# Kernel optimization log

Measured on AMD Instinct MI355X. Metric: run time of the kernel, lower is better.

Reference implementation:

```python
import jax, jax.numpy as jnp
import numpy as np

N_NODES = 50000
N_EDGES = 800000
CH = 128
N_GRAPHS = 8
ADD_TO_EDGE_SCORE = 0.5


def edge_scores(x, row, col, lin_w, lin_b, n):
    """Raw edge score via Linear([x_row||x_col]) then scatter-softmax over col."""
    C = x.shape[1]
    # split-weight form of cat([x[row], x[col]]) @ W^T + b (avoids the [E,2C] concat)
    raw = x[row] @ lin_w[0, :C] + x[col] @ lin_w[0, C:] + lin_b[0]  # [E]
    mx = jax.ops.segment_max(raw, col, num_segments=n)
    ex = jnp.exp(raw - mx[col])
    den = jax.ops.segment_sum(ex, col, num_segments=n)
    return ex / (den[col] + 1e-16) + ADD_TO_EDGE_SCORE


def greedy_match_cluster(row_np, col_np, score_np, n):
    """Greedy maximal matching in descending-score order + 2-element clustering."""
    perm = np.argsort(-score_np)
    rows = row_np.tolist()
    cols = col_np.tolist()
    used = np.zeros(n, dtype=bool)
    match = np.zeros(len(rows), dtype=bool)
    for e in perm.tolist():
        r = rows[e]
        c = cols[e]
        if not (used[r] or used[c]):
            match[e] = True
            used[r] = True
            used[c] = True
    cluster = np.arange(n)
    cluster[col_np[match]] = row_np[match]
    _, cluster = np.unique(cluster, return_inverse=True)
    return match, cluster


def setup_inputs() -> dict:
    key = jax.random.key(0)
    k1, k2, k3, k4, k5 = jax.random.split(key, 5)
    x = jax.random.normal(k1, (N_NODES, CH), dtype=jnp.float32)
    edge_index = jax.random.randint(k2, (2, N_EDGES), 0, N_NODES)
    batch = jnp.sort(jax.random.randint(k3, (N_NODES,), 0, N_GRAPHS))
    bound = 1.0 / np.sqrt(2 * CH)
    lin_w = jax.random.uniform(k4, (1, 2 * CH), minval=-bound, maxval=bound, dtype=jnp.float32)
    lin_b = jax.random.uniform(k5, (1,), minval=-bound, maxval=bound, dtype=jnp.float32)
    return {"x": x, "edge_index": edge_index, "batch": batch, "lin_w": lin_w, "lin_b": lin_b}


def reference(x, edge_index, batch, lin_w, lin_b):
    n = x.shape[0]
    row, col = edge_index[0], edge_index[1]
    score = edge_scores(x, row, col, lin_w, lin_b, n)  # [E]

    # sequential greedy matching / cluster relabeling (host side, non-differentiable)
    row_np, col_np = np.asarray(row), np.asarray(col)
    match, cluster_np = greedy_match_cluster(row_np, col_np, np.asarray(score), n)
    c = int(cluster_np.max()) + 1
    match_idx = jnp.asarray(np.nonzero(match)[0])
    cluster = jnp.asarray(cluster_np, dtype=jnp.int32)

    # pooled features scaled by the contracted edge's score (1.0 for singletons)
    new_x = jax.ops.segment_sum(x, cluster, num_segments=c)  # [c, C]
    root = cluster[row[match_idx]]
    new_edge_score = jnp.ones((c,), x.dtype).at[root].set(score[match_idx])
    new_x = new_x * new_edge_score[:, None]

    # coalesce(cluster[edge_index]): sort + dedup
    lin_idx = cluster_np[row_np].astype(np.int64) * c + cluster_np[col_np]
    uniq = np.unique(lin_idx)
    new_edge_index = jnp.asarray(np.stack([uniq // c, uniq % c]).astype(np.int32))

    new_batch = jnp.zeros((c,), dtype=batch.dtype).at[cluster].set(batch)
    return new_x, new_edge_index, new_batch, new_edge_score, cluster
```

## Files before the change

### kernel.cpp

```cpp
#include <hip/hip_runtime.h>

typedef unsigned int u32;
typedef unsigned short u16;
typedef unsigned long long u64;

#define CH_ 128

__device__ __forceinline__ u32 f2ord(float f){
  u32 u = __float_as_uint(f);
  return ((int)u < 0) ? ~u : (u | 0x80000000u);
}
__device__ __forceinline__ float ord2f(u32 u){
  return (u & 0x80000000u) ? __uint_as_float(u & 0x7FFFFFFFu) : __uint_as_float(~u);
}
__device__ __forceinline__ u32 ldu32(const u32* p){
  return __hip_atomic_load(p, __ATOMIC_RELAXED, __HIP_MEMORY_SCOPE_AGENT);
}
__device__ __forceinline__ void stu32(u32* p, u32 v){
  __hip_atomic_store(p, v, __ATOMIC_RELAXED, __HIP_MEMORY_SCOPE_AGENT);
}

__global__ void k_init(u32* hdr, u32* mxbits, double* den, u64* sw,
                       int* craw, int* medge, u32* deg, u32* acur,
                       u32* wpos, u32* offarr, u32 ucap, int N, int E){
  int i0 = blockIdx.x*blockDim.x + threadIdx.x;
  int nt = gridDim.x*blockDim.x;
  for (int v = i0; v < N; v += nt){
    mxbits[v]=0u; den[v]=0.0; sw[v]=0ull; craw[v]=v; medge[v]=-1;
    deg[v]=0u; acur[v]=0u; wpos[v]=0u;
    if (ucap) offarr[v] = (u32)v * ucap;
  }
  if (i0 == 0){
    for (int i = 0; i < 64; i++) hdr[i] = 0u;
    hdr[6] = (u32)N;
    offarr[N] = ucap ? (u32)N*ucap : (u32)(2*E);
  }
}

__global__ void k_dots(const float* __restrict__ x, const float* __restrict__ lw,
                       float* __restrict__ s, float* __restrict__ t, int N){
  int wid = threadIdx.x >> 6, lane = threadIdx.x & 63;
  int node = blockIdx.x*4 + wid;
  if (node >= N) return;
  const float* xr = x + (size_t)node*CH_;
  float xa = xr[lane], xb = xr[64+lane];
  float sv = xa*lw[lane]      + xb*lw[64+lane];
  float tv = xa*lw[128+lane]  + xb*lw[192+lane];
  #pragma unroll
  for (int m = 1; m < 64; m <<= 1){ sv += __shfl_xor(sv, m); tv += __shfl_xor(tv, m); }
  if (lane == 0){ s[node]=sv; t[node]=tv; }
}

__global__ void k_rawmax(const float* __restrict__ s, const float* __restrict__ t,
                         const int* __restrict__ row, const int* __restrict__ col,
                         const float* __restrict__ lb, float* __restrict__ rawex,
                         u32* __restrict__ mxbits, u32* __restrict__ rc,
                         u32* __restrict__ deg, u32 ucap, int E){
  float b = lb[0];
  int i0 = blockIdx.x*blockDim.x + threadIdx.x;
  int nt = gridDim.x*blockDim.x;
  for (int e = i0; e < E; e += nt){
    int r = row[e], c = col[e];
    float raw = (s[r] + t[c]) + b;
    rawex[e] = raw;
    atomicMax(&mxbits[c], f2ord(raw));
    rc[e] = ((u32)r << 16) | (u32)c;
    if (!ucap){
      atomicAdd(&deg[r], 1u);
      atomicAdd(&deg[c], 1u);
    }
  }
}

__global__ void k_exden(const int* __restrict__ col, const u32* __restrict__ mxbits,
                        float* __restrict__ rawex, double* __restrict__ den, int E){
  int i0 = blockIdx.x*blockDim.x + threadIdx.x;
  int nt = gridDim.x*blockDim.x;
  for (int e = i0; e < E; e += nt){
    int c = col[e];
    float ex = expf(rawex[e] - ord2f(mxbits[c]));
    rawex[e] = ex;
    atomicAdd(&den[c], (double)ex);
  }
}

__global__ void k_score(const int* __restrict__ col, float* __restrict__ rawex,
                        const double* __restrict__ den, int E){
  int i0 = blockIdx.x*blockDim.x + threadIdx.x;
  int nt = gridDim.x*blockDim.x;
  for (int e = i0; e < E; e += nt)
    rawex[e] = rawex[e]/(float)den[col[e]] + 0.5f;
}

__global__ void scan_p1(const u32* __restrict__ in, u32* __restrict__ out,
                        u32* __restrict__ bsums, const u32* __restrict__ nptr){
  __shared__ u32 sh[256];
  u32 n = *nptr;
  int t = threadIdx.x;
  u32 i = blockIdx.x*256u + (u32)t;
  u32 v = (i < n) ? in[i] : 0u;
  sh[t] = v; __syncthreads();
  for (int o = 1; o < 256; o <<= 1){
    u32 a = (t >= o) ? sh[t-o] : 0u;
    __syncthreads();
    sh[t] += a;
    __syncthreads();
  }
  if (i < n) out[i] = sh[t] - v;
  if (t == 255) bsums[blockIdx.x] = sh[255];
}
__global__ void scan_p2(u32* bsums, u32* total){
  __shared__ u32 sh[256];
  int t = threadIdx.x;
  u32 v = bsums[t];
  sh[t] = v; __syncthreads();
  for (int o = 1; o < 256; o <<= 1){
    u32 a = (t >= o) ? sh[t-o] : 0u;
    __syncthreads();
    sh[t] += a;
    __syncthreads();
  }
  bsums[t] = sh[t] - v;
  if (t == 255 && total) *total = sh[255];
}
__global__ void scan_p3(u32* out, const u32* __restrict__ bsums, const u32* __restrict__ nptr){
  u32 n = *nptr;
  u32 i = blockIdx.x*256u + threadIdx.x;
  if (i < n) out[i] += bsums[blockIdx.x];
}

__global__ void __launch_bounds__(256)
k_scoreadj(const u32* __restrict__ rc, const float* __restrict__ score,
           const u32* __restrict__ offarr, u32* __restrict__ acur,
           u64* __restrict__ adj, u16* __restrict__ adjp,
           u32 ucap, int ce, int E, int N){
  int xcd   = blockIdx.x & 7;
  int chunk = blockIdx.x >> 3;
  int vspan = (N + 7) >> 3;
  int vlo = xcd * vspan;
  int vhi = vlo + vspan; if (vhi > N) vhi = N;
  int ebeg = chunk * ce;
  int eend = ebeg + ce; if (eend > E) eend = E;
  for (int e = ebeg + threadIdx.x; e < eend; e += blockDim.x){
    u32 pk = rc[e];
    int r = (int)(pk >> 16), c = (int)(pk & 0xFFFFu);
    bool wr = (r >= vlo) & (r < vhi);
    bool wc = (c >= vlo) & (c < vhi);
    if (wr | wc){
      u64 k = ((u64)__float_as_uint(score[e]) << 20) | (u64)(0xFFFFFu - (u32)e);
      if (wr){
        u32 slot = atomicAdd(&acur[r], 1u);
        if (!ucap || slot < ucap){
          u32 pr = offarr[r] + slot;
          adj[pr] = k; adjp[pr] = (u16)c;
        }
      }
      if (wc){
        u32 slot = atomicAdd(&acur[c], 1u);
        if (!ucap || slot < ucap){
          u32 pc = offarr[c] + slot;
          adj[pc] = k; adjp[pc] = (u16)r;
        }
      }
    }
  }
}

__global__ void k_adjsort(const u32* __restrict__ offarr, const u32* __restrict__ acur,
                          u64* __restrict__ adj, u16* __restrict__ adjp,
                          u32 ucap, int N){
  __shared__ u64 shk[512];
  __shared__ u32 shp[512];
  int lane = threadIdx.x;
  u32 capn = ucap ? ucap : 0xFFFFFFFFu;
  for (int seg = blockIdx.x; seg < N; seg += gridDim.x){
    u32 base = offarr[seg];
    u32 cnt = acur[seg]; if (cnt > capn) cnt = capn;
    int n = (int)cnt;
    if (n <= 1) continue;
    if (n <= 64){
      u64 v = (lane < n) ? adj[base + lane] : 0ull;
      u32 pr = (lane < n) ? (u32)adjp[base + lane] : 0u;
      #pragma unroll
      for (int k2 = 2; k2 <= 64; k2 <<= 1)
        for (int j = k2 >> 1; j > 0; j >>= 1){
          u64 pv = __shfl_xor(v, j);
          u32 pp = (u32)__shfl_xor((int)pr, j);
          bool up  = ((lane & k2) == 0);
          bool low = ((lane & j) == 0);
          bool take_mx = (up == low);
          bool swap = take_mx ? (pv > v) : (pv < v);
          if (swap){ v = pv; pr = pp; }
        }
      if (lane < n){ adj[base + lane] = v; adjp[base + lane] = (u16)pr; }
    } else {
      int msz = 128; while (msz < n) msz <<= 1;
      for (int i = lane; i < msz; i += 64){
        shk[i] = (i < n) ? adj[base + i] : 0ull;
        shp[i] = (i < n) ? (u32)adjp[base + i] : 0u;
      }
      __syncthreads();
      for (int k2 = 2; k2 <= msz; k2 <<= 1){
        for (int j = k2 >> 1; j > 0; j >>= 1){
          for (int i = lane; i < msz; i += 64){
            int ix = i ^ j;
            if (ix > i){
              u64 a = shk[i], b2 = shk[ix];
              bool desc = ((i & k2) == 0);
              if (desc ? (a < b2) : (a > b2)){
                shk[i] = b2; shk[ix] = a;
                u32 t2 = shp[i]; shp[i] = shp[ix]; shp[ix] = t2;
              }
            }
          }
          __syncthreads();
        }
      }
      for (int i = lane; i < n; i += 64){ adj[base+i] = shk[i]; adjp[base+i] = (u16)shp[i]; }
      __syncthreads();
    }
  }
}

__global__ void k_suitor(const u32* __restrict__ rc, const u32* __restrict__ offarr,
                         const u32* __restrict__ acur,
                         const u64* __restrict__ adj, const u16* __restrict__ adjp,
                         u64* sw, u32* wpos, u32 ucap, int N){
  int i0 = blockIdx.x*blockDim.x + threadIdx.x;
  int nt = gridDim.x*blockDim.x;
  u32 capn = ucap ? ucap : 0xFFFFFFFFu;
  for (int v0 = i0; v0 < N; v0 += nt){
    u32 u = (u32)v0;
    u32 pos = offarr[u];
    u32 cnt = acur[u]; if (cnt > capn) cnt = capn;
    u32 end = pos + cnt;
    while (pos < end){
      u64 k = adj[pos];
      u32 v = (u32)adjp[pos];
      pos++;
      if (sw[v] >= k) continue;
      stu32(&wpos[u], pos);
      u64 old = atomicMax((unsigned long long*)&sw[v], (unsigned long long)k);
      if (old >= k) continue;
      if (old == 0ull) break;
      u32 e2 = 0xFFFFFu - (u32)(old & 0xFFFFFu);
      u32 p2 = rc[e2];
      u = ((p2 >> 16) == v) ? (p2 & 0xFFFFu) : (p2 >> 16);
      u32 st = offarr[u];
      u32 c2 = acur[u]; if (c2 > capn) c2 = capn;
      end = st + c2;
      u32 wp = ldu32(&wpos[u]);
      pos = (wp > st) ? wp : st;
    }
  }
}

__global__ void k_exroot(const u64* __restrict__ sw, const u32* __restrict__ rc,
                         int* __restrict__ craw, int* __restrict__ medge,
                         u32* __restrict__ rf, int N){
  int v = blockIdx.x*blockDim.x + threadIdx.x;
  if (v >= N) return;
  u64 k = sw[v];
  bool iscol = false;
  if (k != 0ull){
    u32 e = 0xFFFFFu - (u32)(k & 0xFFFFFu);
    u32 p = rc[e]; u32 r = p >> 16, c = p & 0xFFFFu;
    if ((u32)v == c && sw[r] == k){
      craw[c] = (int)r; medge[r] = (int)e;
      iscol = (r != c);
    }
  }
  rf[v] = iscol ? 0u : 1u;
}

__global__ void k_clusterzero(const int* __restrict__ craw, const u32* __restrict__ newid,
                              int* __restrict__ clout, float* __restrict__ out, size_t offC,
                              u32* __restrict__ hist, u32* __restrict__ cur2,
                              u32* __restrict__ uniqcnt, int N, int M){
  int i = blockIdx.x*blockDim.x + threadIdx.x;
  if (i < M){ hist[i]=0u; cur2[i]=0u; uniqcnt[i]=0u; }
  if (i < N){
    int cl = (int)newid[craw[i]];
    clout[i] = cl;
    out[offC + i] = (float)cl;
  }
}

__global__ void k_hist(const int* __restrict__ row, const int* __restrict__ clout,
                       u32* __restrict__ hist, int E){
  int i0 = blockIdx.x*blockDim.x + threadIdx.x;
  int nt = gridDim.x*blockDim.x;
  for (int e = i0; e < E; e += nt) atomicAdd(&hist[clout[row[e]]], 1u);
}

__global__ void k_scatter(const int* __restrict__ row, const int* __restrict__ col,
                          const int* __restrict__ clout, const u32* __restrict__ segoff,
                          u32* __restrict__ cur2, u32* __restrict__ ccbuf,
                          const u32* __restrict__ hdr, int E){
  const int P = 4;
  int cnum = (int)hdr[2];
  int span = (cnum + P - 1) / P;
  int i0 = blockIdx.x*blockDim.x + threadIdx.x;
  int nt = gridDim.x*blockDim.x;
  for (int p = 0; p < P; p++){
    int lo = p*span;
    int hi = lo + span; if (hi > cnum) hi = cnum;
    for (int e = i0; e < E; e += nt){
      int cr = clout[row[e]];
      if (cr < lo || cr >= hi) continue;
      u32 pos = segoff[cr] + atomicAdd(&cur2[cr], 1u);
      ccbuf[pos] = (u32)clout[col[e]];
    }
  }
}

__global__ void k_segsort(const u32* __restrict__ hdr, const u32* __restrict__ hist,
                          const u32* __restrict__ segoff, u32* __restrict__ ccbuf,
                          u32* __restrict__ uniqcnt){
  int c = (int)hdr[2];
  __shared__ u32 sh[1024];
  int lane = threadIdx.x;
  for (int seg = blockIdx.x; seg < c; seg += gridDim.x){
    int n = (int)hist[seg];
    if (n <= 0){ if (lane == 0) uniqcnt[seg] = 0u; continue; }
    u32 off = segoff[seg];
    if (n <= 64){
      u32 v = (lane < n) ? ccbuf[off + lane] : 0xFFFFFFFFu;
      #pragma unroll
      for (int k = 2; k <= 64; k <<= 1)
        for (int j = k >> 1; j > 0; j >>= 1){
          u32 p = __shfl_xor(v, j);
          bool up  = ((lane & k) == 0);
          bool low = ((lane & j) == 0);
          u32 mn = v < p ? v : p, mx = v < p ? p : v;
          v = (up == low) ? mn : mx;
        }
      u32 pv = __shfl_up(v, 1);
      bool un = (lane < n) && (lane == 0 || v != pv);
      u64 bal = __ballot(un);
      int cnt = __popcll(bal);
      int rk  = __popcll(bal & ((1ull << lane) - 1ull));
      if (un) ccbuf[off + rk] = v;
      if (lane == 0) uniqcnt[seg] = (u32)cnt;
    } else {
      int nn = n > 1024 ? 1024 : n;
      for (int i = lane; i < nn; i += 64) sh[i] = ccbuf[off + i];
      __syncthreads();
      for (int p = 0; p < nn; p++){
        int st = p & 1;
        for (int i = lane; 2*i + 1 + st < nn; i += 64){
          int a = 2*i + st;
          u32 x0 = sh[a], x1 = sh[a+1];
          if (x0 > x1){ sh[a] = x1; sh[a+1] = x0; }
        }
        __syncthreads();
      }
      if (lane == 0){
        int cnt = 0; u32 prev = 0u;
        for (int i = 0; i < nn; i++){
          u32 xv = sh[i];
          if (i == 0 || xv != prev){ ccbuf[off + cnt] = xv; cnt++; prev = xv; }
        }
        uniqcnt[seg] = (u32)cnt;
      }
      __syncthreads();
    }
  }
}

__global__ void k_out(const u32* __restrict__ hdr, const u32* __restrict__ segoff,
                      const u32* __restrict__ uniqcnt, const u32* __restrict__ uniqoff,
                      const u32* __restrict__ ccbuf, const int* __restrict__ craw,
                      const u32* __restrict__ newid, const int* __restrict__ medge,
                      const int* __restrict__ row, const int* __restrict__ col,
                      const float* __restrict__ score, const int* __restrict__ batch,
                      const float* __restrict__ x, float* __restrict__ out, int N){
  int c = (int)hdr[2]; u32 Ep = hdr[3];
  size_t base = (size_t)c * CH_;
  size_t offB = base + 2ull * (size_t)Ep;
  size_t offS = offB + (size_t)c;
  int gw   = (blockIdx.x*blockDim.x + threadIdx.x) >> 6;
  int lane = threadIdx.x & 63;
  int nw   = (gridDim.x*blockDim.x) >> 6;
  for (int seg = gw; seg < c; seg += nw){
    int cnt = (int)uniqcnt[seg];
    u32 so = segoff[seg], uo = uniqoff[seg];
    for (int j = lane; j < cnt; j += 64){
      u32 cc = ccbuf[so + j];
      out[base + uo + j]              = (float)seg;
      out[base + (size_t)Ep + uo + j] = (float)cc;
    }
  }
  for (int i = gw; i < N; i += nw){
    if (craw[i] != i) continue;
    int j = (int)newid[i];
    int e = medge[i];
    int lo = i, hi = i; float sc = 1.0f;
    if (e >= 0){
      int r = row[e], cc = col[e];
      lo = min(r, cc); hi = max(r, cc);
      sc = score[e];
    }
    float v0 = x[(size_t)lo*CH_ + lane];
    float v1 = x[(size_t)lo*CH_ + 64 + lane];
    if (hi != lo){ v0 += x[(size_t)hi*CH_ + lane]; v1 += x[(size_t)hi*CH_ + 64 + lane]; }
    out[(size_t)j*CH_ + lane]      = v0 * sc;
    out[(size_t)j*CH_ + 64 + lane] = v1 * sc;
    if (lane == 0){
      out[offB + j] = (float)batch[hi];
      out[offS + j] = sc;
    }
  }
}

extern "C" void kernel_launch(void* const* d_in, const int* in_sizes, int n_in,
                              void* d_out, int out_size, void* d_ws, size_t ws_size,
                              hipStream_t stream) {
  const float* x     = (const float*)d_in[0];
  const int*   eidx  = (const int*)d_in[1];
  const int*   batch = (const int*)d_in[2];
  const float* lw    = (const float*)d_in[3];
  const float* lb    = (const float*)d_in[4];

  int N = in_sizes[0] / CH_;
  int E = in_sizes[1] / 2;
  const int* row = eidx;
  const int* col = eidx + E;
  float* out = (float*)d_out;

  char* w = (char*)d_ws;
  size_t off = 0;
  auto carve = [&](size_t bytes) -> void* {
    void* p = w + off;
    off += (bytes + 255) & ~(size_t)255;
    return p;
  };
  u32*    hdr    = (u32*)   carve(256);
  double* den    = (double*)carve((size_t)N*8);
  u64*    sw     = (u64*)   carve((size_t)N*8);
  float*  s      = (float*) carve((size_t)N*4);
  float*  t      = (float*) carve((size_t)N*4);
  float*  rawex  = (float*) carve((size_t)E*4);
  u32*    mxbits = (u32*)   carve((size_t)N*4);
  int*    craw   = (int*)   carve((size_t)N*4);
  u32*    rf     = (u32*)   carve((size_t)N*4);
  u32*    newid  = (u32*)   carve((size_t)N*4);
  int*    medge  = (int*)   carve((size_t)N*4);
  int*    clout  = (int*)   carve((size_t)N*4);
  u32*    rc     = (u32*)   carve((size_t)E*4);
  u32*    deg    = (u32*)   carve((size_t)N*4);
  u32*    acur   = (u32*)   carve((size_t)N*4);
  u32*    wpos   = (u32*)   carve((size_t)N*4);
  u32*    offarr = (u32*)   carve((size_t)(N+1)*4);
  u32*    bsums  = (u32*)   carve(256*4);

  u32 cap = 80;
  size_t adjp_b_bytes = ((size_t)N*cap*2 + 255) & ~(size_t)255;
  size_t adj_b_bytes  = ((size_t)N*cap*8 + 255) & ~(size_t)255;
  bool buckets = (off + adjp_b_bytes + adj_b_bytes + (1u<<20) <= ws_size);
  u16* adjp; u64* adj;
  if (buckets){
    adjp = (u16*)carve((size_t)N*cap*2);
    adj  = (u64*)carve((size_t)N*cap*8);
  } else {
    cap = 0;
    adjp = (u16*)carve((size_t)(2*(size_t)E)*2);
    adj  = (u64*)carve((size_t)(2*(size_t)E)*8);
  }
  char* a = (char*)adj;
  size_t aoff = 0;
  auto acarve = [&](size_t bytes) -> void* {
    void* p = a + aoff;
    aoff += (bytes + 255) & ~(size_t)255;
    return p;
  };
  u32* ccbuf   = (u32*)acarve((size_t)E*4);
  u32* hist    = (u32*)acarve((size_t)(N+64)*4);
  u32* segoff  = (u32*)acarve((size_t)(N+64)*4);
  u32* cur2    = (u32*)acarve((size_t)(N+64)*4);
  u32* uniqcnt = (u32*)acarve((size_t)(N+64)*4);
  u32* uniqoff = (u32*)acarve((size_t)(N+64)*4);
  (void)n_in;

  int nbE = (E + 255) / 256;
  int nbN = (N + 255) / 256;
  int ce  = 4096;
  int kch = (E + ce - 1) / ce;

  k_init<<<512, 256, 0, stream>>>(hdr, mxbits, den, sw, craw, medge, deg, acur,
                                  wpos, offarr, cap, N, E);
  k_dots<<<(N + 3)/4, 256, 0, stream>>>(x, lw, s, t, N);
  k_rawmax<<<nbE, 256, 0, stream>>>(s, t, row, col, lb, rawex, mxbits, rc, deg, cap, E);
  k_exden<<<nbE, 256, 0, stream>>>(col, mxbits, rawex, den, E);
  k_score<<<nbE, 256, 0, stream>>>(col, rawex, den, E);

  if (!buckets){
    scan_p1<<<256, 256, 0, stream>>>(deg, offarr, bsums, &hdr[6]);
    scan_p2<<<1, 256, 0, stream>>>(bsums, &hdr[7]);
    scan_p3<<<256, 256, 0, stream>>>(offarr, bsums, &hdr[6]);
  }

  k_scoreadj<<<8*kch, 256, 0, stream>>>(rc, rawex, offarr, acur, adj, adjp,
                                        cap, ce, E, N);
  k_adjsort<<<4096, 64, 0, stream>>>(offarr, acur, adj, adjp, cap, N);
  k_suitor<<<nbN, 256, 0, stream>>>(rc, offarr, acur, adj, adjp, sw, wpos, cap, N);
  k_exroot<<<nbN, 256, 0, stream>>>(sw, rc, craw, medge, rf, N);

  scan_p1<<<256, 256, 0, stream>>>(rf, newid, bsums, &hdr[6]);
  scan_p2<<<1, 256, 0, stream>>>(bsums, &hdr[2]);
  scan_p3<<<256, 256, 0, stream>>>(newid, bsums, &hdr[6]);

  k_clusterzero<<<(N + 64 + 255)/256, 256, 0, stream>>>(craw, newid, clout, out,
                                                        (size_t)(out_size - N),
                                                        hist, cur2, uniqcnt, N, N + 64);
  k_hist<<<nbE, 256, 0, stream>>>(row, clout, hist, E);

  scan_p1<<<256, 256, 0, stream>>>(hist, segoff, bsums, &hdr[2]);
  scan_p2<<<1, 256, 0, stream>>>(bsums, &hdr[4]);
  scan_p3<<<256, 256, 0, stream>>>(segoff, bsums, &hdr[2]);

  k_scatter<<<nbE, 256, 0, stream>>>(row, col, clout, segoff, cur2, ccbuf, hdr, E);
  k_segsort<<<4096, 64, 0, stream>>>(hdr, hist, segoff, ccbuf, uniqcnt);

  scan_p1<<<256, 256, 0, stream>>>(uniqcnt, uniqoff, bsums, &hdr[2]);
  scan_p2<<<1, 256, 0, stream>>>(bsums, &hdr[3]);
  scan_p3<<<256, 256, 0, stream>>>(uniqoff, bsums, &hdr[2]);

  k_out<<<4096, 256, 0, stream>>>(hdr, segoff, uniqcnt, uniqoff, ccbuf, craw, newid,
                                  medge, row, col, rawex, batch, x, out, N);
}
```

Before: 447.6 us.

## Pack neighbor index into 64-bit adjacency sort key, drop separate adjp array

The 16-bit neighbor id is folded into the low bits of the 64-bit adjacency key. The score is rebased by subtracting 0x3F000000 so that 28 bits of score, 20 bits of edge id and 16 bits of neighbor fit in one word. This removes the parallel u16 adjp array, its loads and stores in scoreadj, adjsort and suitor, and the payload shuffles and swaps in the bitonic sorts. It cuts memory traffic and instructions in the matching phase. The cost is that the score key depends on the score being at least 0.5 and below 2, and on node ids fitting in 16 bits, and root detection now compares keys without the neighbor bits.

```diff
diff --git a/kernel.cpp b/kernel.cpp
--- a/kernel.cpp
+++ b/kernel.cpp
@@ -132,8 +132,7 @@
 __global__ void __launch_bounds__(256)
 k_scoreadj(const u32* __restrict__ rc, const float* __restrict__ score,
            const u32* __restrict__ offarr, u32* __restrict__ acur,
-           u64* __restrict__ adj, u16* __restrict__ adjp,
-           u32 ucap, int ce, int E, int N){
+           u64* __restrict__ adj, u32 ucap, int ce, int E, int N){
   int xcd   = blockIdx.x & 7;
   int chunk = blockIdx.x >> 3;
   int vspan = (N + 7) >> 3;
@@ -141,36 +140,29 @@
   int vhi = vlo + vspan; if (vhi > N) vhi = N;
   int ebeg = chunk * ce;
   int eend = ebeg + ce; if (eend > E) eend = E;
-  for (int e = ebeg + threadIdx.x; e < eend; e += blockDim.x){
+  for (int e = ebeg + (int)threadIdx.x; e < eend; e += 256){
     u32 pk = rc[e];
     int r = (int)(pk >> 16), c = (int)(pk & 0xFFFFu);
     bool wr = (r >= vlo) & (r < vhi);
     bool wc = (c >= vlo) & (c < vhi);
     if (wr | wc){
-      u64 k = ((u64)__float_as_uint(score[e]) << 20) | (u64)(0xFFFFFu - (u32)e);
+      u32 sb = __float_as_uint(score[e]) - 0x3F000000u;
+      u64 kb = ((u64)sb << 36) | ((u64)(0xFFFFFu - (u32)e) << 16);
       if (wr){
         u32 slot = atomicAdd(&acur[r], 1u);
-        if (!ucap || slot < ucap){
-          u32 pr = offarr[r] + slot;
-          adj[pr] = k; adjp[pr] = (u16)c;
-        }
+        if (!ucap || slot < ucap) adj[offarr[r] + slot] = kb | (u32)c;
       }
       if (wc){
         u32 slot = atomicAdd(&acur[c], 1u);
-        if (!ucap || slot < ucap){
-          u32 pc = offarr[c] + slot;
-          adj[pc] = k; adjp[pc] = (u16)r;
-        }
+        if (!ucap || slot < ucap) adj[offarr[c] + slot] = kb | (u32)r;
       }
     }
   }
 }
 
 __global__ void k_adjsort(const u32* __restrict__ offarr, const u32* __restrict__ acur,
-                          u64* __restrict__ adj, u16* __restrict__ adjp,
-                          u32 ucap, int N){
+                          u64* __restrict__ adj, u32 ucap, int N){
   __shared__ u64 shk[512];
-  __shared__ u32 shp[512];
   int lane = threadIdx.x;
   u32 capn = ucap ? ucap : 0xFFFFFFFFu;
   for (int seg = blockIdx.x; seg < N; seg += gridDim.x){
@@ -180,25 +172,19 @@
     if (n <= 1) continue;
     if (n <= 64){
       u64 v = (lane < n) ? adj[base + lane] : 0ull;
-      u32 pr = (lane < n) ? (u32)adjp[base + lane] : 0u;
       #pragma unroll
       for (int k2 = 2; k2 <= 64; k2 <<= 1)
         for (int j = k2 >> 1; j > 0; j >>= 1){
           u64 pv = __shfl_xor(v, j);
-          u32 pp = (u32)__shfl_xor((int)pr, j);
           bool up  = ((lane & k2) == 0);
           bool low = ((lane & j) == 0);
-          bool take_mx = (up == low);
-          bool swap = take_mx ? (pv > v) : (pv < v);
-          if (swap){ v = pv; pr = pp; }
+          u64 mx = v > pv ? v : pv, mn = v > pv ? pv : v;
+          v = (up == low) ? mx : mn;
         }
-      if (lane < n){ adj[base + lane] = v; adjp[base + lane] = (u16)pr; }
+      if (lane < n) adj[base + lane] = v;
     } else {
       int msz = 128; while (msz < n) msz <<= 1;
-      for (int i = lane; i < msz; i += 64){
-        shk[i] = (i < n) ? adj[base + i] : 0ull;
-        shp[i] = (i < n) ? (u32)adjp[base + i] : 0u;
-      }
+      for (int i = lane; i < msz; i += 64) shk[i] = (i < n) ? adj[base + i] : 0ull;
       __syncthreads();
       for (int k2 = 2; k2 <= msz; k2 <<= 1){
         for (int j = k2 >> 1; j > 0; j >>= 1){
@@ -207,24 +193,20 @@
             if (ix > i){
               u64 a = shk[i], b2 = shk[ix];
               bool desc = ((i & k2) == 0);
-              if (desc ? (a < b2) : (a > b2)){
-                shk[i] = b2; shk[ix] = a;
-                u32 t2 = shp[i]; shp[i] = shp[ix]; shp[ix] = t2;
-              }
+              if (desc ? (a < b2) : (a > b2)){ shk[i] = b2; shk[ix] = a; }
             }
           }
           __syncthreads();
         }
       }
-      for (int i = lane; i < n; i += 64){ adj[base+i] = shk[i]; adjp[base+i] = (u16)shp[i]; }
+      for (int i = lane; i < n; i += 64) adj[base+i] = shk[i];
       __syncthreads();
     }
   }
 }
 
 __global__ void k_suitor(const u32* __restrict__ rc, const u32* __restrict__ offarr,
-                         const u32* __restrict__ acur,
-                         const u64* __restrict__ adj, const u16* __restrict__ adjp,
+                         const u32* __restrict__ acur, const u64* __restrict__ adj,
                          u64* sw, u32* wpos, u32 ucap, int N){
   int i0 = blockIdx.x*blockDim.x + threadIdx.x;
   int nt = gridDim.x*blockDim.x;
@@ -236,14 +218,14 @@
     u32 end = pos + cnt;
     while (pos < end){
       u64 k = adj[pos];
-      u32 v = (u32)adjp[pos];
+      u32 v = (u32)(k & 0xFFFFu);
       pos++;
       if (sw[v] >= k) continue;
       stu32(&wpos[u], pos);
       u64 old = atomicMax((unsigned long long*)&sw[v], (unsigned long long)k);
       if (old >= k) continue;
       if (old == 0ull) break;
-      u32 e2 = 0xFFFFFu - (u32)(old & 0xFFFFFu);
+      u32 e2 = 0xFFFFFu - (u32)((old >> 16) & 0xFFFFFu);
       u32 p2 = rc[e2];
       u = ((p2 >> 16) == v) ? (p2 & 0xFFFFu) : (p2 >> 16);
       u32 st = offarr[u];
@@ -263,9 +245,9 @@
   u64 k = sw[v];
   bool iscol = false;
   if (k != 0ull){
-    u32 e = 0xFFFFFu - (u32)(k & 0xFFFFFu);
+    u32 e = 0xFFFFFu - (u32)((k >> 16) & 0xFFFFFu);
     u32 p = rc[e]; u32 r = p >> 16, c = p & 0xFFFFu;
-    if ((u32)v == c && sw[r] == k){
+    if ((u32)v == c && (sw[r] >> 16) == (k >> 16)){
       craw[c] = (int)r; medge[r] = (int)e;
       iscol = (r != c);
     }
@@ -455,17 +437,14 @@
   u32*    bsums  = (u32*)   carve(256*4);
 
   u32 cap = 80;
-  size_t adjp_b_bytes = ((size_t)N*cap*2 + 255) & ~(size_t)255;
-  size_t adj_b_bytes  = ((size_t)N*cap*8 + 255) & ~(size_t)255;
-  bool buckets = (off + adjp_b_bytes + adj_b_bytes + (1u<<20) <= ws_size);
-  u16* adjp; u64* adj;
+  size_t adj_b_bytes = ((size_t)N*cap*8 + 255) & ~(size_t)255;
+  bool buckets = (off + adj_b_bytes + (1u<<20) <= ws_size);
+  u64* adj;
   if (buckets){
-    adjp = (u16*)carve((size_t)N*cap*2);
-    adj  = (u64*)carve((size_t)N*cap*8);
+    adj = (u64*)carve((size_t)N*cap*8);
   } else {
     cap = 0;
-    adjp = (u16*)carve((size_t)(2*(size_t)E)*2);
-    adj  = (u64*)carve((size_t)(2*(size_t)E)*8);
+    adj = (u64*)carve((size_t)(2*(size_t)E)*8);
   }
   char* a = (char*)adj;
   size_t aoff = 0;
@@ -500,10 +479,9 @@
     scan_p3<<<256, 256, 0, stream>>>(offarr, bsums, &hdr[6]);
   }
 
-  k_scoreadj<<<8*kch, 256, 0, stream>>>(rc, rawex, offarr, acur, adj, adjp,
-                                        cap, ce, E, N);
-  k_adjsort<<<4096, 64, 0, stream>>>(offarr, acur, adj, adjp, cap, N);
-  k_suitor<<<nbN, 256, 0, stream>>>(rc, offarr, acur, adj, adjp, sw, wpos, cap, N);
+  k_scoreadj<<<8*kch, 256, 0, stream>>>(rc, rawex, offarr, acur, adj, cap, ce, E, N);
+  k_adjsort<<<4096, 64, 0, stream>>>(offarr, acur, adj, cap, N);
+  k_suitor<<<nbN, 256, 0, stream>>>(rc, offarr, acur, adj, sw, wpos, cap, N);
   k_exroot<<<nbN, 256, 0, stream>>>(sw, rc, craw, medge, rf, N);
 
   scan_p1<<<256, 256, 0, stream>>>(rf, newid, bsums, &hdr[6]);
```

Result: faster. 432.9 us (-3.3%).
